# Kernel tuning notes

Hardware: AMD Instinct MI355X
Metric: run time of the kernel (lower is better)

The kernel has to match this reference:

```python
import jax, jax.numpy as jnp
import numpy as np
from jax import lax

B, P, NB, NF, NC, R = 128, 2048, 2000, 250, 16, 128
LS = NB - NF  # number of simulated bins = len_bins_gensig - 1


def setup_inputs() -> dict:
    key = jax.random.key(0)
    ks = jax.random.split(key, 10)
    return {
        'batched_stim_spat': jax.random.normal(ks[0], (B, P), jnp.float32),
        'stim_time': jax.random.normal(ks[1], (NB,), jnp.float32),
        'batched_initial_spike_section': (jax.random.uniform(ks[2], (B, NF)) < 0.05).astype(jnp.float32),
        'batched_coupling_cells': (jax.random.uniform(ks[3], (B, NC, NB)) < 0.05).astype(jnp.float32),
        'spatial_filter': jax.random.normal(ks[4], (P,), jnp.float32) * 0.02,
        'spatial_bias': jnp.float32(-2.0),
        'stim_timecourse_filter': jax.random.normal(ks[5], (NF,), jnp.float32) * 0.1,
        'feedback_filter': jax.random.normal(ks[6], (NF,), jnp.float32) * 0.05 - 0.02,
        'coupling_filter': jax.random.normal(ks[7], (NC, NF), jnp.float32) * 0.05,
        'u': jax.random.uniform(ks[8], (LS, B, R), jnp.float32),
        'n_repeats': R,
    }


def _corr1d_valid(x, k):
    # torch F.conv1d is cross-correlation; lax conv is too (no kernel flip)
    # x: (n,), k: (m,) -> (n - m + 1,)
    out = lax.conv_general_dilated(x[None, None, :], k[None, None, :], (1,), 'VALID',
                                   dimension_numbers=('NCH', 'OIH', 'NCH'))
    return out[0, 0]


def reference(batched_stim_spat, stim_time, batched_initial_spike_section,
              batched_coupling_cells, spatial_filter, spatial_bias,
              stim_timecourse_filter, feedback_filter, coupling_filter, u, n_repeats):
    nf = stim_timecourse_filter.shape[0]

    # stimulus time component: (n_bins - nf + 1,)
    filt_time = _corr1d_valid(stim_time, stim_timecourse_filter)

    # spatial exp arg for separable linear-spatial GLM:
    # einsum('bpt,p->bt', stim_spat[:,:,None]*filt_time, spatial_filter)
    # factors into outer product of (stim_spat @ spatial_filter) and filt_time
    stim_gensig = (batched_stim_spat @ spatial_filter)[:, None] * filt_time[None, :] + spatial_bias  # (B, T)

    # coupling exp arg: conv1d over all coupled cells -> (B, T)
    coup = lax.conv_general_dilated(batched_coupling_cells, coupling_filter[None, :, :], (1,), 'VALID',
                                    dimension_numbers=('NCH', 'OIH', 'NCH'))[:, 0, :]

    gensig_piece = stim_gensig + coup  # (B, T) with T = n_bins - nf + 1
    len_sim = gensig_piece.shape[1] - 1

    # initial feedback window: last nf spike bins, broadcast over repeats
    batch = batched_stim_spat.shape[0]
    w0 = jnp.broadcast_to(batched_initial_spike_section[:, None, :], (batch, n_repeats, nf)) + 0.0

    def step(window, xs):
        g_t, u_t = xs  # (B,), (B, R)
        fb = jnp.einsum('brk,k->br', window, feedback_filter)
        g = g_t[:, None] + fb
        spike = (u_t < jax.nn.sigmoid(g)).astype(window.dtype)  # Bernoulli(sigmoid(g))
        window = jnp.concatenate([window[:, :, 1:], spike[:, :, None]], axis=2)
        return window, spike

    xs = (jnp.swapaxes(gensig_piece[:, :len_sim], 0, 1), u[:len_sim])  # ((LS,B), (LS,B,R))
    _, spikes = lax.scan(step, w0, xs)  # spikes: (LS, B, R)

    out = jnp.concatenate([w0, jnp.moveaxis(spikes, 0, 2)], axis=2)  # (B, R, n_bins)
    return out
```

## Files before the change

### kernel.cpp

```cpp
#include <hip/hip_runtime.h>
#include <math.h>

#define B_  128
#define P_  2048
#define NB_ 2000
#define NF_ 250
#define NC_ 16
#define R_  128
#define LS_ 1750
#define NT_ 1751
#define BR_ (B_ * R_)
#define H_  16
#define NBLK_ 110

typedef int v4i __attribute__((ext_vector_type(4)));

__device__ __forceinline__ double dsel_ab(double a, double b, unsigned long long m) {
    long long ab = __double_as_longlong(a), bb = __double_as_longlong(b);
    int rlo, rhi;
    asm("v_cndmask_b32 %0, %2, %4, %6\n\t"
        "v_cndmask_b32 %1, %3, %5, %6"
        : "=&v"(rlo), "=&v"(rhi)
        : "v"((int)ab), "v"((int)(ab >> 32)), "v"((int)bb), "v"((int)(bb >> 32)), "s"(m));
    return __longlong_as_double(((long long)(unsigned)rlo) | ((long long)rhi << 32));
}

__device__ __forceinline__ double dand(double t, int m) {
    return __longlong_as_double(__double_as_longlong(t) & (long long)m);
}

__device__ __forceinline__ double rcp1(double b) {
    double r;
    asm("v_rcp_f64 %0, %1" : "=v"(r) : "v"(b));
    r = fma(fma(-b, r, 1.0), r, r);
    return r;
}

__device__ __forceinline__ double logit_fast(float uf) {
    double u = (double)uf;
    double v = 1.0 - u;
    double qd = u * rcp1(v);
    long long bits = __double_as_longlong(qd);
    int e = (int)((bits >> 52) & 0x7FF) - 1023;
    double m = __longlong_as_double((bits & 0xFFFFFFFFFFFFFLL) | 0x3FF0000000000000LL);
    if (m > 1.4142135623730951) { m *= 0.5; e += 1; }
    double s = (m - 1.0) * rcp1(m + 1.0);
    float zf = (float)(s * s);
    float Qf = fmaf(zf, fmaf(zf, fmaf(zf, fmaf(zf,
        0.09090909090909091f, 0.1111111111111111f),
        0.14285714285714285f), 0.2f), 0.3333333333333333f);
    double logm = fma(2.0 * s, (double)(zf * Qf), 2.0 * s);
    return fma((double)e, 0.6931471805599453, logm);
}

__global__ __launch_bounds__(256) void k_pre(const float* __restrict__ st,
                                             const float* __restrict__ stf,
                                             const float* __restrict__ sp,
                                             const float* __restrict__ sf,
                                             double* __restrict__ ft,
                                             double* __restrict__ sdot) {
    if (blockIdx.x < 7) {
        int t = blockIdx.x * 256 + threadIdx.x;
        if (t >= NT_) return;
        double s = 0.0;
        for (int k = 0; k < NF_; ++k) s += (double)st[t + k] * (double)stf[k];
        ft[t] = s;
    } else {
        __shared__ double red[256];
        int b = blockIdx.x - 7;
        double s = 0.0;
        for (int p = threadIdx.x; p < P_; p += 256)
            s += (double)sp[(size_t)b * P_ + p] * (double)sf[p];
        red[threadIdx.x] = s;
        __syncthreads();
        for (int off = 128; off > 0; off >>= 1) {
            if (threadIdx.x < off) red[threadIdx.x] += red[threadIdx.x + off];
            __syncthreads();
        }
        if (threadIdx.x == 0) sdot[b] = red[0];
    }
}

__global__ __launch_bounds__(256) void k_coup(const float* __restrict__ cc,
                                              const float* __restrict__ cf,
                                              const double* __restrict__ sdot,
                                              const double* __restrict__ ft,
                                              const float* __restrict__ bias,
                                              double* __restrict__ gensig) {
    __shared__ __align__(16) float  ccs[NC_ * 512];
    __shared__ __align__(16) double cfs[NC_ * 256];
    __shared__ double red[3][64][4];
    int b = blockIdx.y, t0 = blockIdx.x * 256;
    int tid = threadIdx.x, lane = tid & 63, wv = tid >> 6;

    for (int idx = tid; idx < NC_ * 128; idx += 256) {
        int c = idx >> 7, j4 = (idx & 127) * 4, src = t0 + j4;
        const float* p = cc + ((size_t)b * NC_ + c) * NB_ + src;
        float4 v;
        if (src + 3 < NB_) v = *(const float4*)p;
        else {
            v.x = (src     < NB_) ? p[0] : 0.f;
            v.y = (src + 1 < NB_) ? p[1] : 0.f;
            v.z = (src + 2 < NB_) ? p[2] : 0.f;
            v.w = (src + 3 < NB_) ? p[3] : 0.f;
        }
        *(float4*)&ccs[c * 512 + j4] = v;
    }
    for (int idx = tid; idx < NC_ * 256; idx += 256) {
        int c = idx >> 8, k = idx & 255;
        cfs[idx] = (k < NF_) ? (double)cf[c * NF_ + k] : 0.0;
    }
    __syncthreads();

    double a0 = 0, a1 = 0, a2 = 0, a3 = 0;
    int base = lane * 4;
    for (int c = wv; c < NC_; c += 4) {
        const float*  row  = &ccs[c * 512];
        const double* crow = &cfs[c * 256];
        float4 cur = *(const float4*)&row[base];
        for (int k4 = 0; k4 < 252; k4 += 4) {
            float4 nxt = *(const float4*)&row[base + k4 + 4];
            double e0 = cur.x, e1 = cur.y, e2 = cur.z, e3 = cur.w;
            double e4 = nxt.x, e5 = nxt.y, e6 = nxt.z;
            double c0 = crow[k4], c1 = crow[k4 + 1], c2 = crow[k4 + 2], c3 = crow[k4 + 3];
            a0 += e0 * c0 + e1 * c1 + e2 * c2 + e3 * c3;
            a1 += e1 * c0 + e2 * c1 + e3 * c2 + e4 * c3;
            a2 += e2 * c0 + e3 * c1 + e4 * c2 + e5 * c3;
            a3 += e3 * c0 + e4 * c1 + e5 * c2 + e6 * c3;
            cur = nxt;
        }
    }
    if (wv > 0) {
        red[wv - 1][lane][0] = a0; red[wv - 1][lane][1] = a1;
        red[wv - 1][lane][2] = a2; red[wv - 1][lane][3] = a3;
    }
    __syncthreads();
    if (wv == 0) {
        a0 += red[0][lane][0] + red[1][lane][0] + red[2][lane][0];
        a1 += red[0][lane][1] + red[1][lane][1] + red[2][lane][1];
        a2 += red[0][lane][2] + red[1][lane][2] + red[2][lane][2];
        a3 += red[0][lane][3] + red[1][lane][3] + red[2][lane][3];
        double gb = (double)bias[0];
        double sd = sdot[b];
        double accs[4] = {a0, a1, a2, a3};
        int tb = t0 + base;
        for (int i = 0; i < 4; ++i) {
            int t = tb + i;
            if (t < LS_) gensig[(size_t)b * LS_ + t] = sd * ft[t] + gb + accs[i];
        }
    }
}

__global__ __launch_bounds__(512, 2) void k_scan(const double* __restrict__ gensig,
                                                 const float* __restrict__ u,
                                                 const float* __restrict__ iss,
                                                 const float* __restrict__ ff,
                                                 float* __restrict__ out) {
    __shared__ double farT_all[4][16 * 17];
    __shared__ double luring[2][4][4 * 64];
    int tid = threadIdx.x;
    int wv = tid >> 6, l = tid & 63;
    int swv = wv & 3;
    const bool isPrep = (wv >= 4);
    int gw = blockIdx.x * 4 + swv;
    int b = gw >> 3, rbase = (gw & 7) * 16;
    double* farT = &farT_all[swv][0];

    int lw = l & 15;
    int q  = l >> 4;
    int cn = l >> 2;
    int j  = l & 3;
    int jo = 16 + j;
    int sh4cn = cn * 4;
    int sh4lw = lw * 4;

    const unsigned long long COL0_ = 0x1111111111111111ull;
    const unsigned long long COL1_ = COL0_ << 1;
    const unsigned long long COL2_ = COL0_ << 2;
    const unsigned long long COL3_ = COL0_ << 3;
    const unsigned long long COL01_ = COL0_ | COL1_;

    const double* gs   = gensig + (size_t)b * LS_;
    const float*  up   = u + b * R_ + rbase + cn;
    float*        op   = out + ((size_t)(b * R_ + rbase + cn)) * NB_ + NF_;
    const float*  issb = iss + b * NF_;

    unsigned long long W0 = 0, W1 = 0, W2 = 0, W3 = 0;
    v4i Bf[4][6];
    double tp8 = 0, tp9 = 0, tp10 = 0, tp11 = 0, tp12 = 0, tp13 = 0, tp14 = 0, tp15 = 0;
    double tap7lo = 0, tap7hi = 0;
    double SC1 = 0, SC2 = 0, SC3 = 0, SC4 = 0, SC5 = 0, SC6 = 0, SC7 = 0;
    double Cc0 = 0, Cc1 = 0, Cc2 = 0, Cc3 = 0, Cc4 = 0, Cc5 = 0, Cc6 = 0, Cc7 = 0;
    double thr0 = 0, thr1 = 0, thr2 = 0, thr3 = 0;
    double gprep = 0.0;
    float ur0 = 0.f, ur1 = 0.f, ur2 = 0.f, ur3 = 0.f;

    if (!isPrep) {
        for (int idx = l; idx < 16 * NF_; idx += 64) {
            int c = idx / NF_, k = idx - c * NF_;
            out[((size_t)(b * R_ + rbase + c)) * NB_ + k] = issb[k];
        }
        for (int k = 0; k < NF_; ++k) {
            unsigned long long bit = (issb[k] > 0.5f) ? 1ull : 0ull;
            if      (k <  64) W0 |= bit << k;
            else if (k < 128) W1 |= bit << (k - 64);
            else if (k < 192) W2 |= bit << (k - 128);
            else              W3 |= bit << (k - 192);
        }
        int Bword[4][6][4];
#pragma unroll
        for (int kc = 0; kc < 4; ++kc)
#pragma unroll
            for (int p = 0; p < 6; ++p)
#pragma unroll
                for (int w = 0; w < 4; ++w) Bword[kc][p][w] = 0;
#pragma unroll
        for (int kc = 0; kc < 4; ++kc) {
#pragma unroll
            for (int jj = 0; jj < 16; ++jj) {
                int k = kc * 64 + q * 16 + jj;
                int idx = k - lw;
                long long v = 0;
                if (idx >= 0 && idx < NF_)
                    v = __double2ll_rn((double)ff[idx] * 281474976710656.0);
#pragma unroll
                for (int p = 0; p < 6; ++p) {
                    int d = (int)((v + 128) & 255) - 128;
                    v = (v - (long long)d) >> 8;
                    Bword[kc][p][jj >> 2] |= (d & 255) << ((jj & 3) * 8);
                }
            }
        }
#pragma unroll
        for (int kc = 0; kc < 4; ++kc)
#pragma unroll
            for (int p = 0; p < 6; ++p) {
                v4i t; t.x = Bword[kc][p][0]; t.y = Bword[kc][p][1];
                t.z = Bword[kc][p][2]; t.w = Bword[kc][p][3];
                Bf[kc][p] = t;
            }
        double T1d = (double)ff[249], T2d = (double)ff[248], T3d = (double)ff[247];
        double T4d = (double)ff[246], T5d = (double)ff[245], T6d = (double)ff[244];
        double T7d = (double)ff[243];
        tp8  = (double)ff[242]; tp9  = (double)ff[241];
        tp10 = (double)ff[240]; tp11 = (double)ff[239]; tp12 = (double)ff[238];
        tp13 = (double)ff[237]; tp14 = (double)ff[236]; tp15 = (double)ff[235];
        tap7lo = (j < 3) ? T7d : 0.0;
        tap7hi = (j == 3) ? T7d : 0.0;
        SC1 = T1d; SC2 = T2d; SC3 = T1d + T2d;
        SC4 = T3d; SC5 = T3d + T1d; SC6 = T3d + T2d; SC7 = (T3d + T2d) + T1d;
        Cc0 = 0.0; Cc1 = T4d; Cc2 = T5d; Cc3 = T4d + T5d;
        Cc4 = T6d; Cc5 = T6d + T4d; Cc6 = T6d + T5d; Cc7 = (T6d + T5d) + T4d;
    } else {
        ur0 = up[(size_t)(0  + j) * BR_];
        ur1 = up[(size_t)(4  + j) * BR_];
        ur2 = up[(size_t)(8  + j) * BR_];
        ur3 = up[(size_t)(12 + j) * BR_];
        luring[0][swv][  0 + l] = logit_fast(ur0);
        luring[0][swv][ 64 + l] = logit_fast(ur1);
        luring[0][swv][128 + l] = logit_fast(ur2);
        luring[0][swv][192 + l] = logit_fast(ur3);
        ur0 = up[(size_t)(16 + j) * BR_];
        ur1 = up[(size_t)(20 + j) * BR_];
        ur2 = up[(size_t)(24 + j) * BR_];
        ur3 = up[(size_t)(28 + j) * BR_];
        luring[1][swv][  0 + l] = logit_fast(ur0);
        luring[1][swv][ 64 + l] = logit_fast(ur1);
        luring[1][swv][128 + l] = logit_fast(ur2);
        luring[1][swv][192 + l] = logit_fast(ur3);
        ur0 = up[(size_t)(32 + j) * BR_];
        ur1 = up[(size_t)(36 + j) * BR_];
        ur2 = up[(size_t)(40 + j) * BR_];
        ur3 = up[(size_t)(44 + j) * BR_];
    }

    auto do_far = [&](double gp) {
        unsigned long long Sarr[4] = {W0, W1, W2, W3};
        v4i accm[6];
#pragma unroll
        for (int p = 0; p < 6; ++p) accm[p] = (v4i){0, 0, 0, 0};
#pragma unroll
        for (int kc = 0; kc < 4; ++kc) {
            unsigned f = (unsigned)((Sarr[kc] >> (q * 16)) & 0xFFFFull);
            v4i av;
            av.x = (int)((((f      ) & 0xFu) * 0x00204081u) & 0x01010101u);
            av.y = (int)((((f >>  4) & 0xFu) * 0x00204081u) & 0x01010101u);
            av.z = (int)((((f >>  8) & 0xFu) * 0x00204081u) & 0x01010101u);
            av.w = (int)((((f >> 12) & 0xFu) * 0x00204081u) & 0x01010101u);
#pragma unroll
            for (int p = 0; p < 6; ++p)
                accm[p] = __builtin_amdgcn_mfma_i32_16x16x64_i8(av, Bf[kc][p], accm[p], 0, 0, 0);
        }
#pragma unroll
        for (int r = 0; r < 4; ++r) {
            int lo = accm[0][r] + accm[1][r] * 256 + accm[2][r] * 65536;
            int hi = accm[3][r] + accm[4][r] * 256 + accm[5][r] * 65536;
            double fb = gp + (double)lo * 0x1p-48 + (double)hi * 0x1p-24;
            farT[(q * 4 + r) * 17 + lw] = fb;
        }
    };

    auto xb78 = [&](int e4, unsigned q16v) -> double {
        unsigned qs = (q16v << 16) >> e4;
        double x = (dand(tap7lo, __builtin_amdgcn_sbfe((int)qs, jo - 7,  1)) +
                    dand(tp8,  __builtin_amdgcn_sbfe((int)qs, jo - 8,  1))) +
                   (dand(tp9,  __builtin_amdgcn_sbfe((int)qs, jo - 9,  1)) +
                    dand(tp10, __builtin_amdgcn_sbfe((int)qs, jo - 10, 1)));
        double y = (dand(tp11, __builtin_amdgcn_sbfe((int)qs, jo - 11, 1)) +
                    dand(tp12, __builtin_amdgcn_sbfe((int)qs, jo - 12, 1))) +
                   (dand(tp13, __builtin_amdgcn_sbfe((int)qs, jo - 13, 1)) +
                    dand(tp14, __builtin_amdgcn_sbfe((int)qs, jo - 14, 1)));
        return (x + y) + dand(tp15, __builtin_amdgcn_sbfe((int)qs, jo - 15, 1));
    };

    __syncthreads();

    if (!isPrep) {
        gprep = gs[lw];
        do_far(gprep);
        double lu0 = luring[0][swv][  0 + l];
        double lu1 = luring[0][swv][ 64 + l];
        double lu2 = luring[0][swv][128 + l];
        double lu3 = luring[0][swv][192 + l];
        __asm__ volatile("s_waitcnt lgkmcnt(0)" ::: "memory");
        thr0 = lu0 - farT[cn * 17 +  0 + j];
        thr1 = lu1 - farT[cn * 17 +  4 + j];
        thr2 = lu2 - farT[cn * 17 +  8 + j];
        thr3 = lu3 - farT[cn * 17 + 12 + j];
        { int tg = 16 + lw; if (tg > LS_ - 1) tg = LS_ - 1; gprep = gs[tg]; }
    }

    __syncthreads();

#define ROUND(PRE2, SOUT) { \
    double u0_ = dsel_ab(Cc0, Cc1, A4); \
    double u1_ = dsel_ab(Cc2, Cc3, A4); \
    double u2_ = dsel_ab(Cc4, Cc5, A4); \
    double u3_ = dsel_ab(Cc6, Cc7, A4); \
    double v0_ = dsel_ab(u0_, u1_, A5); \
    double v1_ = dsel_ab(u2_, u3_, A5); \
    double sel_ = dsel_ab(v0_, v1_, A6); \
    double rhs_ = (PRE2) - sel_; \
    unsigned long long Bm0 = __ballot(0.0 > rhs_); \
    unsigned long long Bm1 = __ballot(SC1 > rhs_); \
    unsigned long long Bm2 = __ballot(SC2 > rhs_); \
    unsigned long long Bm3 = __ballot(SC3 > rhs_); \
    unsigned long long Bm4 = __ballot(SC4 > rhs_); \
    unsigned long long Bm5 = __ballot(SC5 > rhs_); \
    unsigned long long Bm6 = __ballot(SC6 > rhs_); \
    unsigned long long Bm7 = __ballot(SC7 > rhs_); \
    unsigned long long a3p = P >> 1, a2p = P >> 2; \
    unsigned long long C0 = Bm0 ^ (a3p & (Bm4 ^ Bm0)); \
    unsigned long long C1 = Bm1 ^ (a3p & (Bm5 ^ Bm1)); \
    unsigned long long C2 = Bm2 ^ (a3p & (Bm6 ^ Bm2)); \
    unsigned long long C3 = Bm3 ^ (a3p & (Bm7 ^ Bm3)); \
    unsigned long long D0 = C0 ^ (a2p & (C2 ^ C0)); \
    unsigned long long D1 = C1 ^ (a2p & (C3 ^ C1)); \
    unsigned long long Dd = D1 ^ D0; \
    unsigned long long S = (D0 ^ ((P >> 3) & Dd)) & COL0_; \
    S |= (D0 ^ ((S << 1) & Dd)) & COL1_; \
    { unsigned long long a2s = S << 2; \
      unsigned long long D0b = C0 ^ (a2s & (C2 ^ C0)); \
      unsigned long long D1b = C1 ^ (a2s & (C3 ^ C1)); \
      S |= (D0b ^ ((S << 1) & (D1b ^ D0b))) & COL2_; } \
    { unsigned long long a3s = S << 3, a2s = S << 2; \
      unsigned long long C0c = Bm0 ^ (a3s & (Bm4 ^ Bm0)); \
      unsigned long long C1c = Bm1 ^ (a3s & (Bm5 ^ Bm1)); \
      unsigned long long C2c = Bm2 ^ (a3s & (Bm6 ^ Bm2)); \
      unsigned long long C3c = Bm3 ^ (a3s & (Bm7 ^ Bm3)); \
      unsigned long long D0c = C0c ^ (a2s & (C2c ^ C0c)); \
      unsigned long long D1c = C1c ^ (a2s & (C3c ^ C1c)); \
      S |= (D0c ^ ((S << 1) & (D1c ^ D0c))) & COL3_; } \
    (SOUT) = S; \
    A4 = S; \
    A5 = ((S << 1) & ~COL0_) | ((P >> 3) & COL0_); \
    A6 = ((S << 2) & ~COL01_) | ((P >> 2) & COL01_); \
    P = S; \
}

    int blk = 0;
    for (int t0 = 0; t0 < LS_; t0 += H_, ++blk) {
        if (!isPrep) {
            unsigned long long P = 0, A4 = 0, A5 = 0, A6 = 0;
            unsigned long long S0s, S1s, S2s, S3s;
            ROUND(thr0, S0s)
            unsigned nib0 = ((unsigned)(S0s >> sh4cn)) & 15u;
            unsigned q16 = nib0;
            double d7_1 = dand(tap7hi, -(int)(nib0 & 1u));
            double pre2 = thr2 - xb78(8, q16);
            ROUND(thr1 - d7_1, S1s)
            unsigned nib1 = ((unsigned)(S1s >> sh4cn)) & 15u;
            q16 |= nib1 << 4;
            double d7_2 = dand(tap7hi, -(int)(nib1 & 1u));
            double pre3 = thr3 - xb78(12, q16);
            ROUND(pre2 - d7_2, S2s)
            unsigned nib2 = ((unsigned)(S2s >> sh4cn)) & 15u;
            q16 |= nib2 << 8;
            double d7_3 = dand(tap7hi, -(int)(nib2 & 1u));
            ROUND(pre3 - d7_3, S3s)
            unsigned nib3 = ((unsigned)(S3s >> sh4cn)) & 15u;
            q16 |= nib3 << 12;
            unsigned q2 = q16;

            int rem = LS_ - t0; if (rem > H_) rem = H_;
            int s0 = 4 * j;
            if (s0 + 3 < rem) {
                float4 o;
                o.x = (float)((q2 >> (s0    )) & 1u);
                o.y = (float)((q2 >> (s0 + 1)) & 1u);
                o.z = (float)((q2 >> (s0 + 2)) & 1u);
                o.w = (float)((q2 >> (s0 + 3)) & 1u);
                *(float4*)(op + t0 + s0) = o;
            } else {
#pragma unroll
                for (int e = 0; e < 4; ++e)
                    if (s0 + e < rem) op[t0 + s0 + e] = (float)((q2 >> (s0 + e)) & 1u);
            }

            if (t0 + H_ < LS_) {
                unsigned q2n32 = (((unsigned)(S0s >> sh4lw)) & 15u)
                               | ((((unsigned)(S1s >> sh4lw)) & 15u) << 4)
                               | ((((unsigned)(S2s >> sh4lw)) & 15u) << 8)
                               | ((((unsigned)(S3s >> sh4lw)) & 15u) << 12);

                double lu0 = luring[(blk + 1) & 1][swv][  0 + l];
                double lu1 = luring[(blk + 1) & 1][swv][ 64 + l];
                double lu2 = luring[(blk + 1) & 1][swv][128 + l];
                double lu3 = luring[(blk + 1) & 1][swv][192 + l];

                unsigned long long q2n = (unsigned long long)q2n32;
                W0 = (W0 >> 16) | (W1 << 48);
                W1 = (W1 >> 16) | (W2 << 48);
                W2 = (W2 >> 16) | (W3 << 48);
                W3 = (W3 >> 16) | (q2n << 42);

                do_far(gprep);
                __asm__ volatile("s_waitcnt lgkmcnt(0)" ::: "memory");
                thr0 = lu0 - farT[cn * 17 +  0 + j];
                thr1 = lu1 - farT[cn * 17 +  4 + j];
                thr2 = lu2 - farT[cn * 17 +  8 + j];
                thr3 = lu3 - farT[cn * 17 + 12 + j];

                int tg = t0 + 32 + lw; if (tg > LS_ - 1) tg = LS_ - 1;
                gprep = gs[tg];
            }
        } else {
            if (blk <= NBLK_ - 3) {
                double lu0 = logit_fast(ur0), lu1 = logit_fast(ur1);
                double lu2 = logit_fast(ur2), lu3 = logit_fast(ur3);
                luring[blk & 1][swv][  0 + l] = lu0;
                luring[blk & 1][swv][ 64 + l] = lu1;
                luring[blk & 1][swv][128 + l] = lu2;
                luring[blk & 1][swv][192 + l] = lu3;
                if (blk <= NBLK_ - 4) {
                    int T = (blk + 3) * H_;
                    int t_;
                    t_ = T +  0 + j; if (t_ > LS_ - 1) t_ = LS_ - 1; ur0 = up[(size_t)t_ * BR_];
                    t_ = T +  4 + j; if (t_ > LS_ - 1) t_ = LS_ - 1; ur1 = up[(size_t)t_ * BR_];
                    t_ = T +  8 + j; if (t_ > LS_ - 1) t_ = LS_ - 1; ur2 = up[(size_t)t_ * BR_];
                    t_ = T + 12 + j; if (t_ > LS_ - 1) t_ = LS_ - 1; ur3 = up[(size_t)t_ * BR_];
                }
            }
        }
        __syncthreads();
    }
#undef ROUND
}

extern "C" void kernel_launch(void* const* d_in, const int* in_sizes, int n_in,
                              void* d_out, int out_size, void* d_ws, size_t ws_size,
                              hipStream_t stream) {
    const float* stim_spat = (const float*)d_in[0];
    const float* stim_time = (const float*)d_in[1];
    const float* iss       = (const float*)d_in[2];
    const float* cc        = (const float*)d_in[3];
    const float* sf        = (const float*)d_in[4];
    const float* bias      = (const float*)d_in[5];
    const float* stf       = (const float*)d_in[6];
    const float* ff        = (const float*)d_in[7];
    const float* cf        = (const float*)d_in[8];
    const float* u         = (const float*)d_in[9];
    (void)in_sizes; (void)n_in; (void)out_size; (void)ws_size;

    float* out = (float*)d_out;

    double* ws     = (double*)d_ws;
    double* gensig = ws;
    double* ft     = gensig + (size_t)B_ * LS_;
    double* sdot   = ft + NT_;

    k_pre  <<<135, 256, 0, stream>>>(stim_time, stf, stim_spat, sf, ft, sdot);
    k_coup <<<dim3(7, B_), 256, 0, stream>>>(cc, cf, sdot, ft, bias, gensig);
    k_scan <<<B_ * 2, 512, 0, stream>>>(gensig, u, iss, ff, out);
}
```

Before: 516.7 us.

## Process two 16-step blocks per barrier with a six-slot logit ring

The scan loop now handles two 16-step sub-blocks per iteration, so the workgroup barrier between compute and prep waves fires half as often. The logit ring in LDS grows from 2 to 6 slots, and the prep waves produce and prefetch two blocks per iteration, keeping a deeper lead over the compute waves. The barrier after the prologue is removed. This costs more LDS and registers and makes the slot indexing more complex, with some risk of races or occupancy loss.

Result: faster. 489.5 us (-5.3%).

```diff
diff --git a/kernel.cpp b/kernel.cpp
--- a/kernel.cpp
+++ b/kernel.cpp
@@ -11,7 +11,7 @@
 #define NT_ 1751
 #define BR_ (B_ * R_)
 #define H_  16
-#define NBLK_ 110
+#define NIT_ 55
 
 typedef int v4i __attribute__((ext_vector_type(4)));
 
@@ -157,7 +157,7 @@
                                                  const float* __restrict__ ff,
                                                  float* __restrict__ out) {
     __shared__ double farT_all[4][16 * 17];
-    __shared__ double luring[2][4][4 * 64];
+    __shared__ double luring[6][4][4 * 64];
     int tid = threadIdx.x;
     int wv = tid >> 6, l = tid & 63;
     int swv = wv & 3;
@@ -193,7 +193,10 @@
     double Cc0 = 0, Cc1 = 0, Cc2 = 0, Cc3 = 0, Cc4 = 0, Cc5 = 0, Cc6 = 0, Cc7 = 0;
     double thr0 = 0, thr1 = 0, thr2 = 0, thr3 = 0;
     double gprep = 0.0;
-    float ur0 = 0.f, ur1 = 0.f, ur2 = 0.f, ur3 = 0.f;
+    int rA = 1, rB = 2;
+    float uA0 = 0.f, uA1 = 0.f, uA2 = 0.f, uA3 = 0.f;
+    float uB0 = 0.f, uB1 = 0.f, uB2 = 0.f, uB3 = 0.f;
+    int sA = 4, sB = 5;
 
     if (!isPrep) {
         for (int idx = l; idx < 16 * NF_; idx += 64) {
@@ -252,26 +255,35 @@
         Cc0 = 0.0; Cc1 = T4d; Cc2 = T5d; Cc3 = T4d + T5d;
         Cc4 = T6d; Cc5 = T6d + T4d; Cc6 = T6d + T5d; Cc7 = (T6d + T5d) + T4d;
     } else {
-        ur0 = up[(size_t)(0  + j) * BR_];
-        ur1 = up[(size_t)(4  + j) * BR_];
-        ur2 = up[(size_t)(8  + j) * BR_];
-        ur3 = up[(size_t)(12 + j) * BR_];
-        luring[0][swv][  0 + l] = logit_fast(ur0);
-        luring[0][swv][ 64 + l] = logit_fast(ur1);
-        luring[0][swv][128 + l] = logit_fast(ur2);
-        luring[0][swv][192 + l] = logit_fast(ur3);
-        ur0 = up[(size_t)(16 + j) * BR_];
-        ur1 = up[(size_t)(20 + j) * BR_];
-        ur2 = up[(size_t)(24 + j) * BR_];
-        ur3 = up[(size_t)(28 + j) * BR_];
-        luring[1][swv][  0 + l] = logit_fast(ur0);
-        luring[1][swv][ 64 + l] = logit_fast(ur1);
-        luring[1][swv][128 + l] = logit_fast(ur2);
-        luring[1][swv][192 + l] = logit_fast(ur3);
-        ur0 = up[(size_t)(32 + j) * BR_];
-        ur1 = up[(size_t)(36 + j) * BR_];
-        ur2 = up[(size_t)(40 + j) * BR_];
-        ur3 = up[(size_t)(44 + j) * BR_];
+        float x0, x1, x2, x3, y0, y1, y2, y3;
+        x0 = up[(size_t)(0  + j) * BR_];  x1 = up[(size_t)(4  + j) * BR_];
+        x2 = up[(size_t)(8  + j) * BR_];  x3 = up[(size_t)(12 + j) * BR_];
+        y0 = up[(size_t)(16 + j) * BR_];  y1 = up[(size_t)(20 + j) * BR_];
+        y2 = up[(size_t)(24 + j) * BR_];  y3 = up[(size_t)(28 + j) * BR_];
+        luring[0][swv][  0 + l] = logit_fast(x0);
+        luring[0][swv][ 64 + l] = logit_fast(x1);
+        luring[0][swv][128 + l] = logit_fast(x2);
+        luring[0][swv][192 + l] = logit_fast(x3);
+        luring[1][swv][  0 + l] = logit_fast(y0);
+        luring[1][swv][ 64 + l] = logit_fast(y1);
+        luring[1][swv][128 + l] = logit_fast(y2);
+        luring[1][swv][192 + l] = logit_fast(y3);
+        x0 = up[(size_t)(32 + j) * BR_];  x1 = up[(size_t)(36 + j) * BR_];
+        x2 = up[(size_t)(40 + j) * BR_];  x3 = up[(size_t)(44 + j) * BR_];
+        y0 = up[(size_t)(48 + j) * BR_];  y1 = up[(size_t)(52 + j) * BR_];
+        y2 = up[(size_t)(56 + j) * BR_];  y3 = up[(size_t)(60 + j) * BR_];
+        luring[2][swv][  0 + l] = logit_fast(x0);
+        luring[2][swv][ 64 + l] = logit_fast(x1);
+        luring[2][swv][128 + l] = logit_fast(x2);
+        luring[2][swv][192 + l] = logit_fast(x3);
+        luring[3][swv][  0 + l] = logit_fast(y0);
+        luring[3][swv][ 64 + l] = logit_fast(y1);
+        luring[3][swv][128 + l] = logit_fast(y2);
+        luring[3][swv][192 + l] = logit_fast(y3);
+        uA0 = up[(size_t)(64 + j) * BR_]; uA1 = up[(size_t)(68 + j) * BR_];
+        uA2 = up[(size_t)(72 + j) * BR_]; uA3 = up[(size_t)(76 + j) * BR_];
+        uB0 = up[(size_t)(80 + j) * BR_]; uB1 = up[(size_t)(84 + j) * BR_];
+        uB2 = up[(size_t)(88 + j) * BR_]; uB3 = up[(size_t)(92 + j) * BR_];
     }
 
     auto do_far = [&](double gp) {
@@ -327,10 +339,8 @@
         thr1 = lu1 - farT[cn * 17 +  4 + j];
         thr2 = lu2 - farT[cn * 17 +  8 + j];
         thr3 = lu3 - farT[cn * 17 + 12 + j];
-        { int tg = 16 + lw; if (tg > LS_ - 1) tg = LS_ - 1; gprep = gs[tg]; }
-    }
-
-    __syncthreads();
+        gprep = gs[16 + lw];
+    }
 
 #define ROUND(PRE2, SOUT) { \
     double u0_ = dsel_ab(Cc0, Cc1, A4); \
@@ -378,89 +388,105 @@
     P = S; \
 }
 
-    int blk = 0;
-    for (int t0 = 0; t0 < LS_; t0 += H_, ++blk) {
+    auto sub = [&](int t0s, int rslot, bool more) {
+        unsigned long long P = 0, A4 = 0, A5 = 0, A6 = 0;
+        unsigned long long S0s, S1s, S2s, S3s;
+        ROUND(thr0, S0s)
+        unsigned nib0 = ((unsigned)(S0s >> sh4cn)) & 15u;
+        unsigned q16 = nib0;
+        double d7_1 = dand(tap7hi, -(int)(nib0 & 1u));
+        double pre2 = thr2 - xb78(8, q16);
+        ROUND(thr1 - d7_1, S1s)
+        unsigned nib1 = ((unsigned)(S1s >> sh4cn)) & 15u;
+        q16 |= nib1 << 4;
+        double d7_2 = dand(tap7hi, -(int)(nib1 & 1u));
+        double pre3 = thr3 - xb78(12, q16);
+        ROUND(pre2 - d7_2, S2s)
+        unsigned nib2 = ((unsigned)(S2s >> sh4cn)) & 15u;
+        q16 |= nib2 << 8;
+        double d7_3 = dand(tap7hi, -(int)(nib2 & 1u));
+        ROUND(pre3 - d7_3, S3s)
+        unsigned nib3 = ((unsigned)(S3s >> sh4cn)) & 15u;
+        q16 |= nib3 << 12;
+        unsigned q2 = q16;
+
+        int rem = LS_ - t0s; if (rem > H_) rem = H_;
+        int s0 = 4 * j;
+        if (s0 + 3 < rem) {
+            float4 o;
+            o.x = (float)((q2 >> (s0    )) & 1u);
+            o.y = (float)((q2 >> (s0 + 1)) & 1u);
+            o.z = (float)((q2 >> (s0 + 2)) & 1u);
+            o.w = (float)((q2 >> (s0 + 3)) & 1u);
+            *(float4*)(op + t0s + s0) = o;
+        } else {
+#pragma unroll
+            for (int e = 0; e < 4; ++e)
+                if (s0 + e < rem) op[t0s + s0 + e] = (float)((q2 >> (s0 + e)) & 1u);
+        }
+
+        if (more) {
+            unsigned q2n32 = (((unsigned)(S0s >> sh4lw)) & 15u)
+                           | ((((unsigned)(S1s >> sh4lw)) & 15u) << 4)
+                           | ((((unsigned)(S2s >> sh4lw)) & 15u) << 8)
+                           | ((((unsigned)(S3s >> sh4lw)) & 15u) << 12);
+
+            double lu0 = luring[rslot][swv][  0 + l];
+            double lu1 = luring[rslot][swv][ 64 + l];
+            double lu2 = luring[rslot][swv][128 + l];
+            double lu3 = luring[rslot][swv][192 + l];
+
+            unsigned long long q2n = (unsigned long long)q2n32;
+            W0 = (W0 >> 16) | (W1 << 48);
+            W1 = (W1 >> 16) | (W2 << 48);
+            W2 = (W2 >> 16) | (W3 << 48);
+            W3 = (W3 >> 16) | (q2n << 42);
+
+            do_far(gprep);
+            __asm__ volatile("s_waitcnt lgkmcnt(0)" ::: "memory");
+            thr0 = lu0 - farT[cn * 17 +  0 + j];
+            thr1 = lu1 - farT[cn * 17 +  4 + j];
+            thr2 = lu2 - farT[cn * 17 +  8 + j];
+            thr3 = lu3 - farT[cn * 17 + 12 + j];
+
+            int tg = t0s + 32 + lw; if (tg > LS_ - 1) tg = LS_ - 1;
+            gprep = gs[tg];
+        }
+    };
+
+    for (int it = 0; it < NIT_; ++it) {
         if (!isPrep) {
-            unsigned long long P = 0, A4 = 0, A5 = 0, A6 = 0;
-            unsigned long long S0s, S1s, S2s, S3s;
-            ROUND(thr0, S0s)
-            unsigned nib0 = ((unsigned)(S0s >> sh4cn)) & 15u;
-            unsigned q16 = nib0;
-            double d7_1 = dand(tap7hi, -(int)(nib0 & 1u));
-            double pre2 = thr2 - xb78(8, q16);
-            ROUND(thr1 - d7_1, S1s)
-            unsigned nib1 = ((unsigned)(S1s >> sh4cn)) & 15u;
-            q16 |= nib1 << 4;
-            double d7_2 = dand(tap7hi, -(int)(nib1 & 1u));
-            double pre3 = thr3 - xb78(12, q16);
-            ROUND(pre2 - d7_2, S2s)
-            unsigned nib2 = ((unsigned)(S2s >> sh4cn)) & 15u;
-            q16 |= nib2 << 8;
-            double d7_3 = dand(tap7hi, -(int)(nib2 & 1u));
-            ROUND(pre3 - d7_3, S3s)
-            unsigned nib3 = ((unsigned)(S3s >> sh4cn)) & 15u;
-            q16 |= nib3 << 12;
-            unsigned q2 = q16;
-
-            int rem = LS_ - t0; if (rem > H_) rem = H_;
-            int s0 = 4 * j;
-            if (s0 + 3 < rem) {
-                float4 o;
-                o.x = (float)((q2 >> (s0    )) & 1u);
-                o.y = (float)((q2 >> (s0 + 1)) & 1u);
-                o.z = (float)((q2 >> (s0 + 2)) & 1u);
-                o.w = (float)((q2 >> (s0 + 3)) & 1u);
-                *(float4*)(op + t0 + s0) = o;
-            } else {
-#pragma unroll
-                for (int e = 0; e < 4; ++e)
-                    if (s0 + e < rem) op[t0 + s0 + e] = (float)((q2 >> (s0 + e)) & 1u);
+            sub(32 * it,      rA, true);
+            sub(32 * it + 16, rB, it < 54);
+            rA += 2; if (rA >= 6) rA -= 6;
+            rB += 2; if (rB >= 6) rB -= 6;
+        } else {
+            int TL0 = (2 * it + 6) * H_;
+            int t_;
+            float na0, na1, na2, na3, nb0, nb1, nb2, nb3;
+            t_ = TL0 +  0 + j; if (t_ > LS_ - 1) t_ = LS_ - 1; na0 = up[(size_t)t_ * BR_];
+            t_ = TL0 +  4 + j; if (t_ > LS_ - 1) t_ = LS_ - 1; na1 = up[(size_t)t_ * BR_];
+            t_ = TL0 +  8 + j; if (t_ > LS_ - 1) t_ = LS_ - 1; na2 = up[(size_t)t_ * BR_];
+            t_ = TL0 + 12 + j; if (t_ > LS_ - 1) t_ = LS_ - 1; na3 = up[(size_t)t_ * BR_];
+            t_ = TL0 + 16 + j; if (t_ > LS_ - 1) t_ = LS_ - 1; nb0 = up[(size_t)t_ * BR_];
+            t_ = TL0 + 20 + j; if (t_ > LS_ - 1) t_ = LS_ - 1; nb1 = up[(size_t)t_ * BR_];
+            t_ = TL0 + 24 + j; if (t_ > LS_ - 1) t_ = LS_ - 1; nb2 = up[(size_t)t_ * BR_];
+            t_ = TL0 + 28 + j; if (t_ > LS_ - 1) t_ = LS_ - 1; nb3 = up[(size_t)t_ * BR_];
+
+            if (it <= 52) {
+                luring[sA][swv][  0 + l] = logit_fast(uA0);
+                luring[sA][swv][ 64 + l] = logit_fast(uA1);
+                luring[sA][swv][128 + l] = logit_fast(uA2);
+                luring[sA][swv][192 + l] = logit_fast(uA3);
+                luring[sB][swv][  0 + l] = logit_fast(uB0);
+                luring[sB][swv][ 64 + l] = logit_fast(uB1);
+                luring[sB][swv][128 + l] = logit_fast(uB2);
+                luring[sB][swv][192 + l] = logit_fast(uB3);
             }
-
-            if (t0 + H_ < LS_) {
-                unsigned q2n32 = (((unsigned)(S0s >> sh4lw)) & 15u)
-                               | ((((unsigned)(S1s >> sh4lw)) & 15u) << 4)
-                               | ((((unsigned)(S2s >> sh4lw)) & 15u) << 8)
-                               | ((((unsigned)(S3s >> sh4lw)) & 15u) << 12);
-
-                double lu0 = luring[(blk + 1) & 1][swv][  0 + l];
-                double lu1 = luring[(blk + 1) & 1][swv][ 64 + l];
-                double lu2 = luring[(blk + 1) & 1][swv][128 + l];
-                double lu3 = luring[(blk + 1) & 1][swv][192 + l];
-
-                unsigned long long q2n = (unsigned long long)q2n32;
-                W0 = (W0 >> 16) | (W1 << 48);
-                W1 = (W1 >> 16) | (W2 << 48);
-                W2 = (W2 >> 16) | (W3 << 48);
-                W3 = (W3 >> 16) | (q2n << 42);
-
-                do_far(gprep);
-                __asm__ volatile("s_waitcnt lgkmcnt(0)" ::: "memory");
-                thr0 = lu0 - farT[cn * 17 +  0 + j];
-                thr1 = lu1 - farT[cn * 17 +  4 + j];
-                thr2 = lu2 - farT[cn * 17 +  8 + j];
-                thr3 = lu3 - farT[cn * 17 + 12 + j];
-
-                int tg = t0 + 32 + lw; if (tg > LS_ - 1) tg = LS_ - 1;
-                gprep = gs[tg];
-            }
-        } else {
-            if (blk <= NBLK_ - 3) {
-                double lu0 = logit_fast(ur0), lu1 = logit_fast(ur1);
-                double lu2 = logit_fast(ur2), lu3 = logit_fast(ur3);
-                luring[blk & 1][swv][  0 + l] = lu0;
-                luring[blk & 1][swv][ 64 + l] = lu1;
-                luring[blk & 1][swv][128 + l] = lu2;
-                luring[blk & 1][swv][192 + l] = lu3;
-                if (blk <= NBLK_ - 4) {
-                    int T = (blk + 3) * H_;
-                    int t_;
-                    t_ = T +  0 + j; if (t_ > LS_ - 1) t_ = LS_ - 1; ur0 = up[(size_t)t_ * BR_];
-                    t_ = T +  4 + j; if (t_ > LS_ - 1) t_ = LS_ - 1; ur1 = up[(size_t)t_ * BR_];
-                    t_ = T +  8 + j; if (t_ > LS_ - 1) t_ = LS_ - 1; ur2 = up[(size_t)t_ * BR_];
-                    t_ = T + 12 + j; if (t_ > LS_ - 1) t_ = LS_ - 1; ur3 = up[(size_t)t_ * BR_];
-                }
-            }
+            uA0 = na0; uA1 = na1; uA2 = na2; uA3 = na3;
+            uB0 = nb0; uB1 = nb1; uB2 = nb2; uB3 = nb3;
+            sA += 2; if (sA >= 6) sA -= 6;
+            sB += 2; if (sB >= 6) sB -= 6;
         }
         __syncthreads();
     }
```
